# Kernel optimization log

Measured on AMD Instinct MI355X. Metric: run time of the kernel, lower is better.

The kernel has to match this reference:

```python
import jax, jax.numpy as jnp
import numpy as np

RES_SAMPLE = [-0.4, -0.3, -0.2, -0.1, 0.0, 0.1, 0.2, 0.3, 0.4]
GROUP_NUM = 8


def setup_inputs() -> dict:
    key = jax.random.key(0)
    k1, k2, k3, k4 = jax.random.split(key, 4)
    B, C, H, W = 4, 32, 256, 256
    return {
        "feat_ref": jax.random.normal(k1, (B, C, H, W), dtype=jnp.float32),
        "feat_ls": jax.random.normal(k2, (B, C, H, W), dtype=jnp.float32),
        "feat_rs": jax.random.normal(k3, (B, C, H, W), dtype=jnp.float32),
        "disp_init": jax.random.uniform(k4, (B, 1, H, W), dtype=jnp.float32),
    }


def _bilerp_chw(feat, x, y):
    """Bilinear sample feat [C,H,W] at pixel coords x,y [H,W], zeros padding
    (matches F.grid_sample(mode='bilinear', padding_mode='zeros'))."""
    C, H, W = feat.shape
    x0 = jnp.floor(x); y0 = jnp.floor(y)
    x1 = x0 + 1.0;     y1 = y0 + 1.0
    wx1 = x - x0; wx0 = 1.0 - wx1
    wy1 = y - y0; wy0 = 1.0 - wy1

    def gather(yi, xi):
        valid = (yi >= 0) & (yi <= H - 1) & (xi >= 0) & (xi <= W - 1)
        yc = jnp.clip(yi, 0, H - 1).astype(jnp.int32)
        xc = jnp.clip(xi, 0, W - 1).astype(jnp.int32)
        return feat[:, yc, xc] * valid.astype(feat.dtype)  # [C,H,W]

    return (gather(y0, x0) * (wy0 * wx0)
            + gather(y0, x1) * (wy0 * wx1)
            + gather(y1, x0) * (wy1 * wx0)
            + gather(y1, x1) * (wy1 * wx1))


def _warp_all_disp(feat, disp, x_dist):
    """feat [B,C,H,W], disp [B,D,H,W] -> warped [B,C,D,H,W] (y_dist=0)."""
    B, C, H, W = feat.shape
    xx = jnp.arange(W, dtype=feat.dtype)[None, :] * jnp.ones((H, 1), feat.dtype)  # [H,W]
    yy = jnp.arange(H, dtype=feat.dtype)[:, None] * jnp.ones((1, W), feat.dtype)  # [H,W]

    def per_b(feat_b, disp_b):  # feat_b [C,H,W], disp_b [D,H,W]
        x = xx[None] + x_dist * disp_b                      # [D,H,W]
        y = jnp.broadcast_to(yy, x.shape)                   # [D,H,W]
        return jax.vmap(lambda xs, ys: _bilerp_chw(feat_b, xs, ys))(x, y)  # [D,C,H,W]

    out = jax.vmap(per_b)(feat, disp)                       # [B,D,C,H,W]
    return out.transpose(0, 2, 1, 3, 4)                     # [B,C,D,H,W]


def reference(feat_ref, feat_ls, feat_rs, disp_init):
    B, C, H, W = feat_ref.shape
    res = jnp.asarray(RES_SAMPLE, dtype=feat_ref.dtype)     # [D]
    D = res.shape[0]
    disp = disp_init[:, 0][:, None] + res[None, :, None, None]  # [B,D,H,W]

    warp_left = _warp_all_disp(feat_ls, disp, 1.0)          # [B,C,D,H,W]
    warp_right = _warp_all_disp(feat_rs, disp, -1.0)        # [B,C,D,H,W]
    fr = feat_ref[:, :, None]                                # [B,C,1,H,W]

    mu = (warp_left + warp_right + fr) / 3.0
    var = ((warp_left - mu) ** 2 + (warp_right - mu) ** 2 + (fr - mu) ** 2) / 3.0

    cpg = C // GROUP_NUM
    cost = var.reshape(B, GROUP_NUM, cpg, D, H, W).mean(axis=2)  # [B,G,D,H,W]
    return cost
```

## Files before the change

### kernel.cpp

```cpp
#include <hip/hip_runtime.h>


#define B_ 4
#define C_ 32
#define H_ 256
#define W_ 256
#define D_ 9
#define G_ 8
#define CPG 4
#define HW_ (H_ * W_)

__constant__ float c_res[9] = {-0.4f, -0.3f, -0.2f, -0.1f, 0.0f,
                                0.1f,  0.2f,  0.3f,  0.4f};

__global__ __launch_bounds__(256) void cost_volume_kernel(
    const float* __restrict__ fref,
    const float* __restrict__ fls,
    const float* __restrict__ frs,
    const float* __restrict__ disp0,
    float* __restrict__ out)
{
    int bid = blockIdx.x;
    int g = bid & (G_ - 1);
    int t = bid >> 3;
    int h = t & (H_ - 1);
    int b = t >> 8;
    int w = threadIdx.x;

    float dbase = disp0[((size_t)b * H_ + h) * W_ + w];

    int i0l = (int)floorf((float)w + (dbase + c_res[0]));
    int i0r = (int)floorf((float)w - (dbase + c_res[8]));

    float wl0v[D_], wl1v[D_], wr0v[D_], wr1v[D_];
    int jl[D_], jr[D_];
    #pragma unroll
    for (int d = 0; d < D_; ++d) {
        float disp = dbase + c_res[d];
        float xl = (float)w + disp;
        float fl = floorf(xl);
        float w1 = xl - fl;
        wl1v[d] = w1;
        wl0v[d] = 1.0f - w1;
        jl[d] = (int)fl - i0l;

        float xr = (float)w - disp;
        float fr_ = floorf(xr);
        float w1r = xr - fr_;
        wr1v[d] = w1r;
        wr0v[d] = 1.0f - w1r;
        jr[d] = (int)fr_ - i0r;
    }

    size_t rowbase = ((size_t)b * C_ + g * CPG) * (size_t)HW_ + (size_t)h * W_;
    const float* refrow = fref + rowbase;
    const float* lsrow  = fls  + rowbase;
    const float* rsrow  = frs  + rowbase;

    float acc[D_];
    #pragma unroll
    for (int d = 0; d < D_; ++d) acc[d] = 0.0f;

    #pragma unroll
    for (int cc = 0; cc < CPG; ++cc) {
        int coff = cc * HW_;
        float fr = refrow[coff + w];
        float tl[3], tr[3];
        #pragma unroll
        for (int k = 0; k < 3; ++k) {
            int il = i0l + k;
            tl[k] = (il >= 0 && il < W_) ? lsrow[coff + il] : 0.0f;
            int ir = i0r + k;
            tr[k] = (ir >= 0 && ir < W_) ? rsrow[coff + ir] : 0.0f;
        }
        #pragma unroll
        for (int d = 0; d < D_; ++d) {
            float la = jl[d] ? tl[1] : tl[0];
            float lb = jl[d] ? tl[2] : tl[1];
            float wl = la * wl0v[d] + lb * wl1v[d];
            float ra = jr[d] ? tr[1] : tr[0];
            float rb = jr[d] ? tr[2] : tr[1];
            float wr = ra * wr0v[d] + rb * wr1v[d];
            float mu = (wl + wr + fr) * (1.0f / 3.0f);
            float da = wl - mu;
            float db = wr - mu;
            float dc = fr - mu;
            acc[d] += da * da + db * db + dc * dc;
        }
    }

    size_t obase = ((size_t)(b * G_ + g) * D_) * HW_ + (size_t)h * W_ + w;
    #pragma unroll
    for (int d = 0; d < D_; ++d) {
        out[obase + (size_t)d * HW_] = acc[d] * (1.0f / 12.0f);
    }
}

extern "C" void kernel_launch(void* const* d_in, const int* in_sizes, int n_in,
                              void* d_out, int out_size, void* d_ws, size_t ws_size,
                              hipStream_t stream) {
    const float* fref  = (const float*)d_in[0];
    const float* fls   = (const float*)d_in[1];
    const float* frs   = (const float*)d_in[2];
    const float* disp0 = (const float*)d_in[3];
    float* out = (float*)d_out;

    dim3 grid(B_ * H_ * G_);
    dim3 block(W_);
    cost_volume_kernel<<<grid, block, 0, stream>>>(fref, fls, frs, disp0, out);
}
```

Measured before the change: 166.5 us.

## Process all groups per block with precomputed tap weights and packed FP32 math

```diff
diff --git a/kernel.cpp b/kernel.cpp
--- a/kernel.cpp
+++ b/kernel.cpp
@@ -10,8 +10,7 @@
 #define CPG 4
 #define HW_ (H_ * W_)
 
-__constant__ float c_res[9] = {-0.4f, -0.3f, -0.2f, -0.1f, 0.0f,
-                                0.1f,  0.2f,  0.3f,  0.4f};
+typedef float v2f __attribute__((ext_vector_type(2)));
 
 __global__ __launch_bounds__(256) void cost_volume_kernel(
     const float* __restrict__ fref,
@@ -20,79 +19,101 @@
     const float* __restrict__ disp0,
     float* __restrict__ out)
 {
-    int bid = blockIdx.x;
-    int g = bid & (G_ - 1);
-    int t = bid >> 3;
+    const float res[D_] = {-0.4f, -0.3f, -0.2f, -0.1f, 0.0f,
+                            0.1f,  0.2f,  0.3f,  0.4f};
+    int t = blockIdx.x;
     int h = t & (H_ - 1);
     int b = t >> 8;
     int w = threadIdx.x;
 
     float dbase = disp0[((size_t)b * H_ + h) * W_ + w];
 
-    int i0l = (int)floorf((float)w + (dbase + c_res[0]));
-    int i0r = (int)floorf((float)w - (dbase + c_res[8]));
+    int i0l = (int)floorf((float)w + (dbase + res[0]));
+    int i0r = (int)floorf((float)w - (dbase + res[8]));
 
-    float wl0v[D_], wl1v[D_], wr0v[D_], wr1v[D_];
-    int jl[D_], jr[D_];
+    float vl[3], vr[3];
+    int il[3], ir[3];
+    #pragma unroll
+    for (int k = 0; k < 3; ++k) {
+        int a = i0l + k;
+        vl[k] = (a >= 0 && a < W_) ? 1.0f : 0.0f;
+        il[k] = min(max(a, 0), W_ - 1);
+        int c = i0r + k;
+        vr[k] = (c >= 0 && c < W_) ? 1.0f : 0.0f;
+        ir[k] = min(max(c, 0), W_ - 1);
+    }
+
+    float la[D_], lb[D_], lc[D_];
+    float ra[D_], rb[D_], rc[D_];
     #pragma unroll
     for (int d = 0; d < D_; ++d) {
-        float disp = dbase + c_res[d];
+        float disp = dbase + res[d];
+
         float xl = (float)w + disp;
         float fl = floorf(xl);
         float w1 = xl - fl;
-        wl1v[d] = w1;
-        wl0v[d] = 1.0f - w1;
-        jl[d] = (int)fl - i0l;
+        float w0 = 1.0f - w1;
+        bool jl = ((int)fl != i0l);
+        la[d] = jl ? 0.0f : w0 * vl[0];
+        lb[d] = jl ? w0 * vl[1] : w1 * vl[1];
+        lc[d] = jl ? w1 * vl[2] : 0.0f;
 
         float xr = (float)w - disp;
-        float fr_ = floorf(xr);
-        float w1r = xr - fr_;
-        wr1v[d] = w1r;
-        wr0v[d] = 1.0f - w1r;
-        jr[d] = (int)fr_ - i0r;
+        float fx = floorf(xr);
+        float u1 = xr - fx;
+        float u0 = 1.0f - u1;
+        bool jr = ((int)fx != i0r);
+        ra[d] = jr ? 0.0f : u0 * vr[0];
+        rb[d] = jr ? u0 * vr[1] : u1 * vr[1];
+        rc[d] = jr ? u1 * vr[2] : 0.0f;
     }
 
-    size_t rowbase = ((size_t)b * C_ + g * CPG) * (size_t)HW_ + (size_t)h * W_;
-    const float* refrow = fref + rowbase;
-    const float* lsrow  = fls  + rowbase;
-    const float* rsrow  = frs  + rowbase;
+    size_t base = (size_t)b * C_ * HW_ + (size_t)h * W_;
+    const float* pref = fref + base;
+    const float* pls  = fls  + base;
+    const float* prs  = frs  + base;
 
-    float acc[D_];
-    #pragma unroll
-    for (int d = 0; d < D_; ++d) acc[d] = 0.0f;
+    size_t obase = (size_t)b * G_ * D_ * HW_ + (size_t)h * W_ + w;
 
-    #pragma unroll
-    for (int cc = 0; cc < CPG; ++cc) {
-        int coff = cc * HW_;
-        float fr = refrow[coff + w];
-        float tl[3], tr[3];
+    #pragma unroll 1
+    for (int g = 0; g < G_; ++g) {
+        v2f acc[D_];
         #pragma unroll
-        for (int k = 0; k < 3; ++k) {
-            int il = i0l + k;
-            tl[k] = (il >= 0 && il < W_) ? lsrow[coff + il] : 0.0f;
-            int ir = i0r + k;
-            tr[k] = (ir >= 0 && ir < W_) ? rsrow[coff + ir] : 0.0f;
+        for (int d = 0; d < D_; ++d) acc[d] = (v2f)(0.0f);
+
+        #pragma unroll
+        for (int p = 0; p < 2; ++p) {
+            size_t c0 = (size_t)(g * CPG + p * 2) * HW_;
+            const float* rrow = pref + c0;
+            const float* lrow = pls + c0;
+            const float* rsw  = prs + c0;
+
+            v2f fr = { rrow[w],      rrow[HW_ + w] };
+            v2f t0 = { lrow[il[0]],  lrow[HW_ + il[0]] };
+            v2f t1 = { lrow[il[1]],  lrow[HW_ + il[1]] };
+            v2f t2 = { lrow[il[2]],  lrow[HW_ + il[2]] };
+            v2f u0 = { rsw[ir[0]],   rsw[HW_ + ir[0]] };
+            v2f u1 = { rsw[ir[1]],   rsw[HW_ + ir[1]] };
+            v2f u2 = { rsw[ir[2]],   rsw[HW_ + ir[2]] };
+
+            v2f fr2 = fr * fr;
+
+            #pragma unroll
+            for (int d = 0; d < D_; ++d) {
+                v2f wl = t0 * la[d] + t1 * lb[d] + t2 * lc[d];
+                v2f wr = u0 * ra[d] + u1 * rb[d] + u2 * rc[d];
+                v2f s  = wl + wr + fr;
+                v2f q  = __builtin_elementwise_fma(
+                             wl, wl, __builtin_elementwise_fma(wr, wr, fr2));
+                acc[d] += q - s * s * (1.0f / 3.0f);
+            }
         }
+
         #pragma unroll
         for (int d = 0; d < D_; ++d) {
-            float la = jl[d] ? tl[1] : tl[0];
-            float lb = jl[d] ? tl[2] : tl[1];
-            float wl = la * wl0v[d] + lb * wl1v[d];
-            float ra = jr[d] ? tr[1] : tr[0];
-            float rb = jr[d] ? tr[2] : tr[1];
-            float wr = ra * wr0v[d] + rb * wr1v[d];
-            float mu = (wl + wr + fr) * (1.0f / 3.0f);
-            float da = wl - mu;
-            float db = wr - mu;
-            float dc = fr - mu;
-            acc[d] += da * da + db * db + dc * dc;
+            float v = (acc[d].x + acc[d].y) * (1.0f / 12.0f);
+            out[obase + (size_t)(g * D_ + d) * HW_] = v;
         }
-    }
-
-    size_t obase = ((size_t)(b * G_ + g) * D_) * HW_ + (size_t)h * W_ + w;
-    #pragma unroll
-    for (int d = 0; d < D_; ++d) {
-        out[obase + (size_t)d * HW_] = acc[d] * (1.0f / 12.0f);
     }
 }
 
@@ -105,7 +126,7 @@
     const float* disp0 = (const float*)d_in[3];
     float* out = (float*)d_out;
 
-    dim3 grid(B_ * H_ * G_);
+    dim3 grid(B_ * H_);
     dim3 block(W_);
     cost_volume_kernel<<<grid, block, 0, stream>>>(fref, fls, frs, disp0, out);
 }
```

Measured after the change: 173.2 us. 4.0% more time.
